# Kernel optimization log

Measured on AMD Instinct MI355X. Metric: run time of the kernel, lower is better.

Reference implementation:

```python
import jax, jax.numpy as jnp
import numpy as np

H = 8  # num_heads
C = 512  # embed_dims
L = 3  # num_layers
SCALE = (C // H) ** -0.5


def _ln(x, g, b, eps=1e-5):
    mu = jnp.mean(x, axis=-1, keepdims=True)
    var = jnp.mean((x - mu) ** 2, axis=-1, keepdims=True)
    return g * (x - mu) / jnp.sqrt(var + eps) + b


def setup_inputs() -> dict:
    key = jax.random.key(0)
    ks = jax.random.split(key, 12)
    B, Nq, Nk = 16, 64, 4096
    s = 0.02
    return dict(
        queries=jax.random.normal(ks[0], (B, Nq, C), jnp.float32),
        feat=jax.random.normal(ks[1], (B, Nk, C), jnp.float32),
        extra_token=jax.random.normal(ks[2], (B, 1, C), jnp.float32),
        Wq=jax.random.normal(ks[3], (L, C, C), jnp.float32) * s,
        bq=jnp.zeros((L, C), jnp.float32),
        Wk=jax.random.normal(ks[4], (L, C, C), jnp.float32) * s,
        bk=jnp.zeros((L, C), jnp.float32),
        Wv=jax.random.normal(ks[5], (L, C, C), jnp.float32) * s,
        bv=jnp.zeros((L, C), jnp.float32),
        Wo=jax.random.normal(ks[6], (L, C, C), jnp.float32) * s,
        bo=jnp.zeros((L, C), jnp.float32),
        W1=jax.random.normal(ks[7], (L, C, 4 * C), jnp.float32) * s,
        b1=jnp.zeros((L, 4 * C), jnp.float32),
        W2=jax.random.normal(ks[8], (L, 4 * C, C), jnp.float32) * s,
        b2=jnp.zeros((L, C), jnp.float32),
        g2=jnp.ones((L, C), jnp.float32),
        beta2=jnp.zeros((L, C), jnp.float32),
        g3=jnp.ones((L, C), jnp.float32),
        beta3=jnp.zeros((L, C), jnp.float32),
    )


def reference(queries, feat, extra_token, Wq, bq, Wk, bk, Wv, bv, Wo, bo,
              W1, b1, W2, b2, g2, beta2, g3, beta3):
    B, Nq, _ = queries.shape
    Nk = feat.shape[1]
    hd = C // H
    # extra gating token is NOT projected through q: raw reshape -> [B,H,1,hd]
    eq = extra_token.reshape(B, 1, H, hd).transpose(0, 2, 1, 3)
    x = queries
    outs, attns, affs = [], [], []
    for i in range(L):
        q = (x @ Wq[i] + bq[i]).reshape(B, Nq, H, hd).transpose(0, 2, 1, 3)
        k = (feat @ Wk[i] + bk[i]).reshape(B, Nk, H, hd).transpose(0, 2, 1, 3)
        v = (feat @ Wv[i] + bv[i]).reshape(B, Nk, H, hd).transpose(0, 2, 1, 3)
        attn = jnp.einsum('bhqd,bhkd->bhqk', q, k) * SCALE  # pre-softmax scores
        # affinity gate from extra token, averaged over heads -> [B,1,1,Nk]
        aff = jax.nn.sigmoid(jnp.mean(
            jnp.einsum('bhod,bhkd->bhok', eq, k) * SCALE, axis=1, keepdims=True))
        p = aff * jax.nn.softmax(attn, axis=-1)  # gated probabilities
        o = jnp.einsum('bhqk,bhkd->bqhd', p, v).reshape(B, Nq, C)
        o = o @ Wo[i] + bo[i]
        x = _ln(x + o, g2[i], beta2[i])
        ff = jax.nn.relu(x @ W1[i] + b1[i]) @ W2[i] + b2[i]
        x = _ln(x + ff, g3[i], beta3[i])
        outs.append(x)
        attns.append(attn.sum(axis=1) / H)  # head-averaged pre-softmax scores
        affs.append(aff)
    return (jnp.stack(outs), jnp.stack(attns), jnp.stack(affs))
```

## Files before the change

kernel.cpp:

```cpp
#include <hip/hip_runtime.h>


typedef unsigned short u16;
typedef __attribute__((ext_vector_type(8))) short short8;
typedef __attribute__((ext_vector_type(4))) short short4v;
typedef __attribute__((ext_vector_type(4))) float f32x4;

__device__ __forceinline__ float b2f(u16 u) {
    union { unsigned int i; float f; } v; v.i = ((unsigned int)u) << 16; return v.f;
}
__device__ __forceinline__ u16 f2b(float f) {
    unsigned int x = __float_as_uint(f);
    x += 0x7fffu + ((x >> 16) & 1u);
    return (u16)(x >> 16);
}

__device__ __forceinline__ float waveSum(float v) {
#pragma unroll
    for (int o = 32; o > 0; o >>= 1) v += __shfl_xor(v, o);
    return v;
}
__device__ __forceinline__ float waveMax(float v) {
#pragma unroll
    for (int o = 32; o > 0; o >>= 1) v = fmaxf(v, __shfl_xor(v, o));
    return v;
}

__device__ __forceinline__ void gl_lds16(const void* g, void* l) {
    __builtin_amdgcn_global_load_lds(
        (__attribute__((address_space(1))) void*)g,
        (__attribute__((address_space(3))) void*)l, 16, 0, 0);
}

template<bool BIAS_ROW, bool AFFC>
__global__ __launch_bounds__(512, 1) void gemm256_bt_k(
    const u16* __restrict__ A, const u16* __restrict__ Bt,
    const float* __restrict__ bias, u16* __restrict__ Cout,
    int lda, int ldb, int ldc, long sA2, long sB2, long sC2,
    const float* __restrict__ affc)
{
    __shared__ u16 As[3][256][64];
    __shared__ u16 Bs[3][128][64];
    const int t = threadIdx.x;
    const int lane = t & 63;
    const int wave = t >> 6;
    const int z = blockIdx.z;
    A  += (long)z * sA2;
    Bt += (long)z * sB2;
    const long cbase = (long)z * sC2;
    const int n0 = blockIdx.x * 128;
    const int m0 = blockIdx.y * 256;
    const int wm = wave >> 1;
    const int wn = wave & 1;
    const int rl = lane & 15, uq = lane >> 4;
    const int srow = lane >> 3;
    const int up   = lane & 7;

    f32x4 acc[4][4];
#pragma unroll
    for (int i = 0; i < 4; ++i)
#pragma unroll
        for (int j = 0; j < 4; ++j) acc[i][j] = (f32x4){0.f, 0.f, 0.f, 0.f};

    auto stage = [&](int buf, int kt) {
        const int k0 = kt * 64;
#pragma unroll
        for (int r = 0; r < 4; ++r) {
            const int row = r * 64 + wave * 8 + srow;
            const int ul = up ^ (row & 7);
            gl_lds16(A + (long)(m0 + row) * lda + k0 + ul * 8,
                     &As[buf][r * 64 + wave * 8][0]);
        }
#pragma unroll
        for (int r = 0; r < 2; ++r) {
            const int row = r * 64 + wave * 8 + srow;
            const int ul = up ^ (row & 7);
            gl_lds16(Bt + (long)(n0 + row) * ldb + k0 + ul * 8,
                     &Bs[buf][r * 64 + wave * 8][0]);
        }
    };

    auto compute = [&](int buf) {
        short8 af[2][4], bf[2][4];
#pragma unroll
        for (int kc = 0; kc < 2; ++kc) {
#pragma unroll
            for (int i = 0; i < 4; ++i) {
                const int R = wm * 64 + i * 16 + rl;
                af[kc][i] = *(const short8*)(&As[buf][R][((kc * 4 + uq) ^ (R & 7)) * 8]);
            }
#pragma unroll
            for (int j = 0; j < 4; ++j) {
                const int R = wn * 64 + j * 16 + rl;
                bf[kc][j] = *(const short8*)(&Bs[buf][R][((kc * 4 + uq) ^ (R & 7)) * 8]);
            }
        }
        __builtin_amdgcn_s_setprio(1);
#pragma unroll
        for (int kc = 0; kc < 2; ++kc)
#pragma unroll
            for (int i = 0; i < 4; ++i)
#pragma unroll
                for (int j = 0; j < 4; ++j)
                    acc[i][j] = __builtin_amdgcn_mfma_f32_16x16x32_bf16(
                        af[kc][i], bf[kc][j], acc[i][j], 0, 0, 0);
        __builtin_amdgcn_s_setprio(0);
    };

    stage(0, 0);
    stage(1, 1);
    asm volatile("s_waitcnt vmcnt(6)\n\ts_barrier" ::: "memory");

#pragma unroll
    for (int kt = 0; kt < 8; ++kt) {
        if (kt + 2 < 8) stage((kt + 2) % 3, kt + 2);
        compute(kt % 3);
        if (kt < 6) {
            asm volatile("s_waitcnt vmcnt(6)\n\ts_barrier" ::: "memory");
        } else if (kt == 6) {
            asm volatile("s_waitcnt vmcnt(0)\n\ts_barrier" ::: "memory");
        }
    }

    const int r0 = (lane >> 4) * 4;
    const int c0 = lane & 15;
#pragma unroll
    for (int i = 0; i < 4; ++i) {
#pragma unroll
        for (int j = 0; j < 4; ++j) {
#pragma unroll
            for (int r = 0; r < 4; ++r) {
                const int row = m0 + wm * 64 + i * 16 + r0 + r;
                const int col = n0 + wn * 64 + j * 16 + c0;
                float v = acc[i][j][r];
                if constexpr (BIAS_ROW) v += bias[row]; else v += bias[col];
                if constexpr (AFFC) v *= affc[(long)z * 4096 + col];
                Cout[cbase + (long)row * ldc + col] = f2b(v);
            }
        }
    }
}

template<int TM, int TN, bool OUT_BF16, bool RELU, bool BIAS_ROW, bool HAS_BIAS,
         bool AFFC, bool SMAX>
__global__ __launch_bounds__(256) void gemm_bt_k(
    const u16* __restrict__ A, const u16* __restrict__ Bt,
    const float* __restrict__ bias, void* __restrict__ Cout,
    int K, int lda, int ldb, int ldc,
    int bdiv, long sA1, long sA2, long sB1, long sB2, long sC1, long sC2,
    float alpha, const float* __restrict__ affc, const float2* __restrict__ stats)
{
    __shared__ u16 As[TM][64];
    __shared__ u16 Bs[TN][64];
    const int t = threadIdx.x;
    const int lane = t & 63;
    const int wave = t >> 6;
    const int z = blockIdx.z;
    const int zq = z / bdiv, zr = z % bdiv;
    A  += (long)zq * sA1 + (long)zr * sA2;
    Bt += (long)zq * sB1 + (long)zr * sB2;
    const long cbase = (long)zq * sC1 + (long)zr * sC2;
    const int n0 = blockIdx.x * TN;
    const int m0 = blockIdx.y * TM;
    constexpr int FM = TM / 32, FN = TN / 32;
    const int wr = wave >> 1, wc = wave & 1;
    const int rl = lane & 15, uq = lane >> 4;

    float2 st[FM];
    if constexpr (SMAX) {
#pragma unroll
        for (int i = 0; i < FM; ++i)
            st[i] = stats[zr * 64 + m0 + wr * (TM / 2) + i * 16 + rl];
    }

    f32x4 acc[FM][FN];
#pragma unroll
    for (int i = 0; i < FM; ++i)
#pragma unroll
        for (int j = 0; j < FN; ++j) acc[i][j] = (f32x4){0.f, 0.f, 0.f, 0.f};

    const int srow = lane >> 3;
    const int up   = lane & 7;

    for (int k0 = 0; k0 < K; k0 += 64) {
        __syncthreads();
#pragma unroll
        for (int r = 0; r < TM / 32; ++r) {
            const int br = (wave * (TM / 32) + r) * 8;
            const int row = br + srow;
            const int ul = up ^ (row & 7);
            gl_lds16(A + (long)(m0 + row) * lda + k0 + ul * 8, &As[br][0]);
        }
#pragma unroll
        for (int r = 0; r < TN / 32; ++r) {
            const int br = (wave * (TN / 32) + r) * 8;
            const int row = br + srow;
            const int ul = up ^ (row & 7);
            gl_lds16(Bt + (long)(n0 + row) * ldb + k0 + ul * 8, &Bs[br][0]);
        }
        __syncthreads();

#pragma unroll
        for (int kc = 0; kc < 2; ++kc) {
            short8 af[FM], bf[FN];
#pragma unroll
            for (int i = 0; i < FM; ++i) {
                const int R = wr * (TM / 2) + i * 16 + rl;
                af[i] = *(const short8*)(&As[R][((kc * 4 + uq) ^ (R & 7)) * 8]);
                if constexpr (SMAX) {
#pragma unroll
                    for (int e = 0; e < 8; ++e)
                        af[i][e] = (short)f2b(
                            __expf(b2f((u16)af[i][e]) - st[i].x) * st[i].y);
                }
            }
#pragma unroll
            for (int j = 0; j < FN; ++j) {
                const int R = wc * (TN / 2) + j * 16 + rl;
                bf[j] = *(const short8*)(&Bs[R][((kc * 4 + uq) ^ (R & 7)) * 8]);
            }
#pragma unroll
            for (int i = 0; i < FM; ++i)
#pragma unroll
                for (int j = 0; j < FN; ++j)
                    acc[i][j] = __builtin_amdgcn_mfma_f32_16x16x32_bf16(
                        af[i], bf[j], acc[i][j], 0, 0, 0);
        }
    }

    const int r0 = (lane >> 4) * 4;
    const int c0 = lane & 15;
#pragma unroll
    for (int i = 0; i < FM; ++i) {
#pragma unroll
        for (int j = 0; j < FN; ++j) {
#pragma unroll
            for (int r = 0; r < 4; ++r) {
                const int row = m0 + wr * (TM / 2) + i * 16 + r0 + r;
                const int col = n0 + wc * (TN / 2) + j * 16 + c0;
                float v = acc[i][j][r] * alpha;
                if constexpr (HAS_BIAS) {
                    if constexpr (BIAS_ROW) v += bias[row]; else v += bias[col];
                }
                if constexpr (AFFC) v *= affc[(long)zq * 4096 + col];
                if constexpr (RELU) v = fmaxf(v, 0.f);
                const long idx = cbase + (long)row * ldc + col;
                if constexpr (OUT_BF16) ((u16*)Cout)[idx] = f2b(v);
                else                    ((float*)Cout)[idx] = v;
            }
        }
    }
}

__global__ __launch_bounds__(256) void smstats_k(
    const u16* __restrict__ S, float2* __restrict__ stats,
    float* __restrict__ attns)
{
    const int bq = blockIdx.x;
    const int b = bq >> 6, q = bq & 63;
    const int t = threadIdx.x;
    const int w = t >> 6, lane = t & 63;
    __shared__ float red[4];
    const int kb = t * 16;

    float attnacc[16];
#pragma unroll
    for (int j = 0; j < 16; ++j) attnacc[j] = 0.f;

    for (int h = 0; h < 8; ++h) {
        const long roff = (((long)(b * 8 + h)) * 64 + q) * 4096;
        const u16* Srow = S + roff;
        float v[16];
        short8 s0 = *(const short8*)(Srow + kb);
        short8 s1 = *(const short8*)(Srow + kb + 8);
#pragma unroll
        for (int j = 0; j < 8; ++j) { v[j] = b2f((u16)s0[j]); v[8 + j] = b2f((u16)s1[j]); }

        float m = -3.0e38f;
#pragma unroll
        for (int j = 0; j < 16; ++j) m = fmaxf(m, v[j]);
        m = waveMax(m);
        __syncthreads();
        if (lane == 0) red[w] = m;
        __syncthreads();
        m = fmaxf(fmaxf(red[0], red[1]), fmaxf(red[2], red[3]));

        float s = 0.f;
#pragma unroll
        for (int j = 0; j < 16; ++j) s += __expf(v[j] - m);
        s = waveSum(s);
        __syncthreads();
        if (lane == 0) red[w] = s;
        __syncthreads();
        s = red[0] + red[1] + red[2] + red[3];

        if (t == 0) stats[(b * 8 + h) * 64 + q] = make_float2(m, 1.f / s);
#pragma unroll
        for (int j = 0; j < 16; ++j) attnacc[j] += v[j];
    }
    float* arow = attns + (long)bq * 4096;
#pragma unroll
    for (int j = 0; j < 16; ++j) arow[kb + j] = attnacc[j] * 0.125f;
}

__global__ __launch_bounds__(256) void pv_reduce_k(
    const float* __restrict__ part, u16* __restrict__ o16)
{
    const int i = blockIdx.x * 256 + threadIdx.x;
    const int d4 = i & 15;
    const int q  = (i >> 4) & 63;
    const int bh = i >> 10;
    const float* p = part + (long)bh * 4096 + q * 64 + d4 * 4;
    float4 s = {0.f, 0.f, 0.f, 0.f};
#pragma unroll
    for (int sp = 0; sp < 8; ++sp) {
        const float4 v = *(const float4*)(p + (long)sp * 524288);
        s.x += v.x; s.y += v.y; s.z += v.z; s.w += v.w;
    }
    const int b = bh >> 3, h = bh & 7;
    u16* o = o16 + (long)b * 32768 + q * 512 + h * 64 + d4 * 4;
    short4v r;
    r[0] = (short)f2b(s.x); r[1] = (short)f2b(s.y);
    r[2] = (short)f2b(s.z); r[3] = (short)f2b(s.w);
    *(short4v*)o = r;
}

__global__ __launch_bounds__(256) void ffred_k(
    const float* __restrict__ part, const float* __restrict__ bias,
    float* __restrict__ out)
{
    const int i = (blockIdx.x * 256 + threadIdx.x) * 4;
    const int c = i & 511;
    float4 s = *(const float4*)(part + i);
#pragma unroll
    for (int sp = 1; sp < 4; ++sp) {
        const float4 v = *(const float4*)(part + (long)sp * 524288 + i);
        s.x += v.x; s.y += v.y; s.z += v.z; s.w += v.w;
    }
    s.x += bias[c]; s.y += bias[c + 1]; s.z += bias[c + 2]; s.w += bias[c + 3];
    *(float4*)(out + i) = s;
}

__global__ __launch_bounds__(256) void umat_k(
    const float* __restrict__ Wk, const float* __restrict__ extra,
    float* __restrict__ u)
{
    __shared__ float ex[16][512];
    const int l = blockIdx.x;
    const int t = threadIdx.x;
    for (int i = t; i < 16 * 512 / 4; i += 256)
        ((float4*)&ex[0][0])[i] = ((const float4*)extra)[i];
    __syncthreads();
    const int lane = t & 63, wave = t >> 6;
    const int row = blockIdx.y * 4 + wave;
    const float* wrow = Wk + ((size_t)l * 512 + row) * 512 + lane * 8;
    float w[8];
#pragma unroll
    for (int j = 0; j < 8; ++j) w[j] = wrow[j];
    float s[16];
#pragma unroll
    for (int b = 0; b < 16; ++b) {
        float x = 0.f;
#pragma unroll
        for (int j = 0; j < 8; ++j) x += w[j] * ex[b][lane * 8 + j];
        s[b] = waveSum(x);
    }
    if (lane < 16) u[((size_t)l * 16 + lane) * 512 + row] = s[lane];
}

__global__ __launch_bounds__(256) void cbk_k(
    const float* __restrict__ bk, const float* __restrict__ extra,
    float* __restrict__ cb)
{
    const int gw = blockIdx.x * 4 + (threadIdx.x >> 6);
    const int lane = threadIdx.x & 63;
    const int l = gw >> 4, b = gw & 15;
    float s = 0.f;
#pragma unroll
    for (int j = 0; j < 8; ++j)
        s += extra[b * 512 + lane * 8 + j] * bk[l * 512 + lane * 8 + j];
    s = waveSum(s);
    if (lane == 0) cb[gw] = s;
}

__global__ __launch_bounds__(256) void cvt16_aff_k(
    const float* __restrict__ feat, u16* __restrict__ dst,
    const float* __restrict__ u, const float* __restrict__ cb,
    float* __restrict__ affb, float* __restrict__ affs_out)
{
    const int t = blockIdx.x * 256 + threadIdx.x;
    const long i = (long)t * 8;
    const int lane = threadIdx.x & 63;
    const int r = t >> 6;
    const int b = r >> 12;
    const float4 a0 = *(const float4*)(feat + i);
    const float4 a1 = *(const float4*)(feat + i + 4);
    short8 o;
    o[0] = (short)f2b(a0.x); o[1] = (short)f2b(a0.y);
    o[2] = (short)f2b(a0.z); o[3] = (short)f2b(a0.w);
    o[4] = (short)f2b(a1.x); o[5] = (short)f2b(a1.y);
    o[6] = (short)f2b(a1.z); o[7] = (short)f2b(a1.w);
    *(short8*)(dst + i) = o;
    const float f[8] = {a0.x, a0.y, a0.z, a0.w, a1.x, a1.y, a1.z, a1.w};
#pragma unroll
    for (int l = 0; l < 3; ++l) {
        const float* ur = u + ((size_t)l * 16 + b) * 512 + lane * 8;
        float s = 0.f;
#pragma unroll
        for (int j = 0; j < 8; ++j) s += f[j] * ur[j];
        s = waveSum(s);
        if (lane == 0) {
            const float av = 1.f / (1.f + __expf(-0.015625f * (s + cb[l * 16 + b])));
            affb[l * 65536 + r] = av;
            affs_out[l * 65536 + r] = av;
        }
    }
}

template<bool WRITE_OUT>
__global__ __launch_bounds__(256) void ln_k(
    float* __restrict__ x, const float* __restrict__ add,
    const float* __restrict__ g, const float* __restrict__ be,
    u16* __restrict__ x16, float* __restrict__ outp)
{
    const int r = blockIdx.x, t = threadIdx.x;
    const int w = t >> 6, lane = t & 63;
    __shared__ float red[4];
    float* xr = x + (long)r * 512;
    const float* ar = add + (long)r * 512;
    const float v0 = xr[2 * t]     + ar[2 * t];
    const float v1 = xr[2 * t + 1] + ar[2 * t + 1];
    float s = waveSum(v0 + v1);
    if (lane == 0) red[w] = s;
    __syncthreads();
    s = red[0] + red[1] + red[2] + red[3];
    const float mu = s * (1.f / 512.f);
    const float d0 = v0 - mu, d1 = v1 - mu;
    __syncthreads();
    float vs = waveSum(d0 * d0 + d1 * d1);
    if (lane == 0) red[w] = vs;
    __syncthreads();
    vs = red[0] + red[1] + red[2] + red[3];
    const float rs = rsqrtf(vs * (1.f / 512.f) + 1e-5f);
    const float o0 = g[2 * t]     * d0 * rs + be[2 * t];
    const float o1 = g[2 * t + 1] * d1 * rs + be[2 * t + 1];
    xr[2 * t] = o0; xr[2 * t + 1] = o1;
    x16[(long)r * 512 + 2 * t]     = f2b(o0);
    x16[(long)r * 512 + 2 * t + 1] = f2b(o1);
    if constexpr (WRITE_OUT) {
        outp[(long)r * 512 + 2 * t]     = o0;
        outp[(long)r * 512 + 2 * t + 1] = o1;
    }
}

__global__ __launch_bounds__(256) void initx_k(
    const float* __restrict__ src, float* __restrict__ x, u16* __restrict__ x16)
{
    const long i = ((long)blockIdx.x * 256 + threadIdx.x) * 8;
    const float4 a = *(const float4*)(src + i);
    const float4 b = *(const float4*)(src + i + 4);
    *(float4*)(x + i) = a;
    *(float4*)(x + i + 4) = b;
    short8 r;
    r[0] = (short)f2b(a.x); r[1] = (short)f2b(a.y); r[2] = (short)f2b(a.z); r[3] = (short)f2b(a.w);
    r[4] = (short)f2b(b.x); r[5] = (short)f2b(b.y); r[6] = (short)f2b(b.z); r[7] = (short)f2b(b.w);
    *(short8*)(x16 + i) = r;
}

__global__ __launch_bounds__(256) void transpose_w_k(
    const float* __restrict__ W, u16* __restrict__ WT, int K, int N)
{
    __shared__ float tile[32][33];
    const int z = blockIdx.z;
    W  += (size_t)z * K * N;
    WT += (size_t)z * K * N;
    const int n0 = blockIdx.x * 32, k0 = blockIdx.y * 32;
    const int tx = threadIdx.x & 31, ty = threadIdx.x >> 5;
#pragma unroll
    for (int j = 0; j < 32; j += 8)
        tile[ty + j][tx] = W[(size_t)(k0 + ty + j) * N + n0 + tx];
    __syncthreads();
#pragma unroll
    for (int j = 0; j < 32; j += 8)
        WT[(size_t)(n0 + ty + j) * K + k0 + tx] = f2b(tile[tx][ty + j]);
}

extern "C" void kernel_launch(void* const* d_in, const int* in_sizes, int n_in,
                              void* d_out, int out_size, void* d_ws, size_t ws_size,
                              hipStream_t stream)
{
    (void)in_sizes; (void)n_in; (void)out_size; (void)ws_size;
    const float* queries = (const float*)d_in[0];
    const float* feat    = (const float*)d_in[1];
    const float* extra   = (const float*)d_in[2];
    const float* Wq = (const float*)d_in[3];  const float* bq = (const float*)d_in[4];
    const float* Wk = (const float*)d_in[5];  const float* bk = (const float*)d_in[6];
    const float* Wv = (const float*)d_in[7];  const float* bv = (const float*)d_in[8];
    const float* Wo = (const float*)d_in[9];  const float* bo = (const float*)d_in[10];
    const float* W1 = (const float*)d_in[11]; const float* b1 = (const float*)d_in[12];
    const float* W2 = (const float*)d_in[13]; const float* b2 = (const float*)d_in[14];
    const float* g2 = (const float*)d_in[15]; const float* be2 = (const float*)d_in[16];
    const float* g3 = (const float*)d_in[17]; const float* be3 = (const float*)d_in[18];

    char* wsb = (char*)d_ws;
    size_t off = 0;
    auto alloc = [&](size_t bytes) -> char* {
        char* p = wsb + off; off += (bytes + 255) & ~(size_t)255; return p;
    };
    u16*  feat16 = (u16*)alloc(33554432ull * 2);
    u16*  WqT = (u16*)alloc(786432ull * 2);
    u16*  WkT = (u16*)alloc(786432ull * 2);
    u16*  WvT = (u16*)alloc(786432ull * 2);
    u16*  WoT = (u16*)alloc(786432ull * 2);
    u16*  W1T = (u16*)alloc(3145728ull * 2);
    u16*  W2T = (u16*)alloc(3145728ull * 2);
    u16*  K16 = (u16*)alloc(33554432ull * 2);
    u16*  VT16 = (u16*)alloc(33554432ull * 2);
    u16*  q16 = (u16*)alloc(524288ull * 2);
    u16*  S16 = (u16*)alloc(33554432ull * 2);
    float* affb  = (float*)alloc(196608ull * 4);
    u16*  o16 = (u16*)alloc(524288ull * 2);
    float* oproj = (float*)alloc(524288ull * 4);
    float* xb    = (float*)alloc(524288ull * 4);
    u16*  x16 = (u16*)alloc(524288ull * 2);
    u16*  h116 = (u16*)alloc(2097152ull * 2);
    float* ffb   = (float*)alloc(524288ull * 4);
    float* uvec  = (float*)alloc(24576ull * 4);
    float* cb    = (float*)alloc(48ull * 4);
    float2* stats = (float2*)alloc(8192ull * 8);
    float* partPV = (float*)K16;
    float* part2  = (float*)VT16;

    float* out_f = (float*)d_out;
    float* outs_base  = out_f;
    float* attns_base = out_f + 1572864;
    float* affs_base  = out_f + 14155776;

    umat_k<<<dim3(3, 128), 256, 0, stream>>>(Wk, extra, uvec);
    cbk_k<<<12, 256, 0, stream>>>(bk, extra, cb);
    cvt16_aff_k<<<16384, 256, 0, stream>>>(feat, feat16, uvec, cb, affb, affs_base);
    initx_k<<<256, 256, 0, stream>>>(queries, xb, x16);
    transpose_w_k<<<dim3(16, 16, 3), 256, 0, stream>>>(Wq, WqT, 512, 512);
    transpose_w_k<<<dim3(16, 16, 3), 256, 0, stream>>>(Wk, WkT, 512, 512);
    transpose_w_k<<<dim3(16, 16, 3), 256, 0, stream>>>(Wv, WvT, 512, 512);
    transpose_w_k<<<dim3(16, 16, 3), 256, 0, stream>>>(Wo, WoT, 512, 512);
    transpose_w_k<<<dim3(64, 16, 3), 256, 0, stream>>>(W1, W1T, 512, 2048);
    transpose_w_k<<<dim3(16, 64, 3), 256, 0, stream>>>(W2, W2T, 2048, 512);

    for (int i = 0; i < 3; ++i) {
        gemm256_bt_k<false, false><<<dim3(4, 256, 1), 512, 0, stream>>>(
            feat16, WkT + i * 262144, bk + i * 512, K16,
            512, 512, 512, 0, 0, 0, nullptr);
        gemm256_bt_k<true, true><<<dim3(32, 2, 16), 512, 0, stream>>>(
            WvT + i * 262144, feat16, bv + i * 512, VT16,
            512, 512, 4096, 0, 2097152, 2097152, affb + i * 65536);
        gemm_bt_k<64, 64, true, false, false, true, false, false>
            <<<dim3(8, 16, 1), 256, 0, stream>>>(
            x16, WqT + i * 262144, bq + i * 512, q16,
            512, 512, 512, 512, 1, 0, 0, 0, 0, 0, 0, 1.f, nullptr, nullptr);
        gemm_bt_k<64, 128, true, false, false, false, false, false>
            <<<dim3(32, 1, 128), 256, 0, stream>>>(
            q16, K16, nullptr, S16,
            64, 512, 512, 4096, 8, 32768, 64, 2097152, 64, 2097152, 262144,
            0.125f, nullptr, nullptr);
        smstats_k<<<1024, 256, 0, stream>>>(
            S16, stats, attns_base + (size_t)i * 4194304);
        gemm_bt_k<64, 64, false, false, false, false, false, true>
            <<<dim3(1, 1, 1024), 256, 0, stream>>>(
            S16, VT16, nullptr, partPV,
            512, 4096, 4096, 64, 128, 512, 262144, 512, 262144, 524288, 4096,
            1.f, nullptr, stats);
        pv_reduce_k<<<512, 256, 0, stream>>>(partPV, o16);
        gemm_bt_k<64, 64, false, false, false, true, false, false>
            <<<dim3(8, 16, 1), 256, 0, stream>>>(
            o16, WoT + i * 262144, bo + i * 512, oproj,
            512, 512, 512, 512, 1, 0, 0, 0, 0, 0, 0, 1.f, nullptr, nullptr);
        ln_k<false><<<1024, 256, 0, stream>>>(xb, oproj, g2 + i * 512, be2 + i * 512, x16, nullptr);
        gemm_bt_k<64, 128, true, true, false, true, false, false>
            <<<dim3(16, 16, 1), 256, 0, stream>>>(
            x16, W1T + (size_t)i * 1048576, b1 + i * 2048, h116,
            512, 512, 512, 2048, 1, 0, 0, 0, 0, 0, 0, 1.f, nullptr, nullptr);
        gemm_bt_k<64, 64, false, false, false, false, false, false>
            <<<dim3(8, 16, 4), 256, 0, stream>>>(
            h116, W2T + (size_t)i * 1048576, nullptr, part2,
            512, 2048, 2048, 512, 1, 512, 0, 512, 0, 524288, 0,
            1.f, nullptr, nullptr);
        ffred_k<<<512, 256, 0, stream>>>(part2, b2 + i * 512, ffb);
        ln_k<true><<<1024, 256, 0, stream>>>(xb, ffb, g3 + i * 512, be3 + i * 512, x16,
                                             outs_base + (size_t)i * 524288);
    }
}
```

Baseline: 816.9 us.

## Enlarge K/V projection GEMM tiles to 256x256 with XCD-aware block remapping

Grows the large K and V projection GEMM output tile from 256x128 to 256x256, with each wave computing a 128x64 sub-tile, so each loaded A/B slice gets more reuse. Pipelining drops from a triple-buffered, partially waited scheme to plain double buffering with __syncthreads, keeping LDS within budget. Block IDs are remapped so that consecutive tiles land on the same XCD, aiming for better L2 locality. In exchange there are more accumulator registers, half as many workgroups, and less latency hiding from the shallower prefetch.

After: 777.3 us. 1.05x faster.

```diff
diff --git a/kernel.cpp b/kernel.cpp
--- a/kernel.cpp
+++ b/kernel.cpp
@@ -32,33 +32,46 @@
         (__attribute__((address_space(3))) void*)l, 16, 0, 0);
 }
 
-template<bool BIAS_ROW, bool AFFC>
-__global__ __launch_bounds__(512, 1) void gemm256_bt_k(
+template<bool BIAS_ROW, bool HAS_BIAS, bool AFFC>
+__global__ __launch_bounds__(512, 1) void gemm256x256_k(
     const u16* __restrict__ A, const u16* __restrict__ Bt,
     const float* __restrict__ bias, u16* __restrict__ Cout,
     int lda, int ldb, int ldc, long sA2, long sB2, long sC2,
     const float* __restrict__ affc)
 {
-    __shared__ u16 As[3][256][64];
-    __shared__ u16 Bs[3][128][64];
+    __shared__ u16 As[2][256][64];
+    __shared__ u16 Bs[2][256][64];
     const int t = threadIdx.x;
     const int lane = t & 63;
     const int wave = t >> 6;
-    const int z = blockIdx.z;
+
+    const int gx = gridDim.x, gy = gridDim.y;
+    const int nwg = gx * gy * gridDim.z;
+    int id;
+    {
+        const int orig = blockIdx.x + blockIdx.y * gx + blockIdx.z * gx * gy;
+        const int qq = nwg >> 3, rr = nwg & 7;
+        const int xcd = orig & 7, sub = orig >> 3;
+        id = (xcd < rr ? xcd * (qq + 1) : rr * (qq + 1) + (xcd - rr) * qq) + sub;
+    }
+    const int bx = id % gx;
+    const int by = (id / gx) % gy;
+    const int z  = id / (gx * gy);
+
     A  += (long)z * sA2;
     Bt += (long)z * sB2;
     const long cbase = (long)z * sC2;
-    const int n0 = blockIdx.x * 128;
-    const int m0 = blockIdx.y * 256;
-    const int wm = wave >> 1;
-    const int wn = wave & 1;
+    const int n0 = bx * 256;
+    const int m0 = by * 256;
+    const int wm = wave >> 2;
+    const int wn = wave & 3;
     const int rl = lane & 15, uq = lane >> 4;
     const int srow = lane >> 3;
     const int up   = lane & 7;
 
-    f32x4 acc[4][4];
-#pragma unroll
-    for (int i = 0; i < 4; ++i)
+    f32x4 acc[8][4];
+#pragma unroll
+    for (int i = 0; i < 8; ++i)
 #pragma unroll
         for (int j = 0; j < 4; ++j) acc[i][j] = (f32x4){0.f, 0.f, 0.f, 0.f};
 
@@ -72,7 +85,7 @@
                      &As[buf][r * 64 + wave * 8][0]);
         }
 #pragma unroll
-        for (int r = 0; r < 2; ++r) {
+        for (int r = 0; r < 4; ++r) {
             const int row = r * 64 + wave * 8 + srow;
             const int ul = up ^ (row & 7);
             gl_lds16(Bt + (long)(n0 + row) * ldb + k0 + ul * 8,
@@ -81,59 +94,55 @@
     };
 
     auto compute = [&](int buf) {
-        short8 af[2][4], bf[2][4];
 #pragma unroll
         for (int kc = 0; kc < 2; ++kc) {
-#pragma unroll
-            for (int i = 0; i < 4; ++i) {
-                const int R = wm * 64 + i * 16 + rl;
-                af[kc][i] = *(const short8*)(&As[buf][R][((kc * 4 + uq) ^ (R & 7)) * 8]);
+            short8 af[8], bf[4];
+#pragma unroll
+            for (int i = 0; i < 8; ++i) {
+                const int R = wm * 128 + i * 16 + rl;
+                af[i] = *(const short8*)(&As[buf][R][((kc * 4 + uq) ^ (R & 7)) * 8]);
             }
 #pragma unroll
             for (int j = 0; j < 4; ++j) {
                 const int R = wn * 64 + j * 16 + rl;
-                bf[kc][j] = *(const short8*)(&Bs[buf][R][((kc * 4 + uq) ^ (R & 7)) * 8]);
+                bf[j] = *(const short8*)(&Bs[buf][R][((kc * 4 + uq) ^ (R & 7)) * 8]);
             }
-        }
-        __builtin_amdgcn_s_setprio(1);
-#pragma unroll
-        for (int kc = 0; kc < 2; ++kc)
-#pragma unroll
-            for (int i = 0; i < 4; ++i)
+            __builtin_amdgcn_s_setprio(1);
+#pragma unroll
+            for (int i = 0; i < 8; ++i)
 #pragma unroll
                 for (int j = 0; j < 4; ++j)
                     acc[i][j] = __builtin_amdgcn_mfma_f32_16x16x32_bf16(
-                        af[kc][i], bf[kc][j], acc[i][j], 0, 0, 0);
-        __builtin_amdgcn_s_setprio(0);
+                        af[i], bf[j], acc[i][j], 0, 0, 0);
+            __builtin_amdgcn_s_setprio(0);
+        }
     };
 
     stage(0, 0);
-    stage(1, 1);
-    asm volatile("s_waitcnt vmcnt(6)\n\ts_barrier" ::: "memory");
-
+    __syncthreads();
+    int buf = 0;
 #pragma unroll
     for (int kt = 0; kt < 8; ++kt) {
-        if (kt + 2 < 8) stage((kt + 2) % 3, kt + 2);
-        compute(kt % 3);
-        if (kt < 6) {
-            asm volatile("s_waitcnt vmcnt(6)\n\ts_barrier" ::: "memory");
-        } else if (kt == 6) {
-            asm volatile("s_waitcnt vmcnt(0)\n\ts_barrier" ::: "memory");
-        }
+        if (kt + 1 < 8) stage(buf ^ 1, kt + 1);
+        compute(buf);
+        __syncthreads();
+        buf ^= 1;
     }
 
     const int r0 = (lane >> 4) * 4;
     const int c0 = lane & 15;
 #pragma unroll
-    for (int i = 0; i < 4; ++i) {
+    for (int i = 0; i < 8; ++i) {
 #pragma unroll
         for (int j = 0; j < 4; ++j) {
 #pragma unroll
             for (int r = 0; r < 4; ++r) {
-                const int row = m0 + wm * 64 + i * 16 + r0 + r;
+                const int row = m0 + wm * 128 + i * 16 + r0 + r;
                 const int col = n0 + wn * 64 + j * 16 + c0;
                 float v = acc[i][j][r];
-                if constexpr (BIAS_ROW) v += bias[row]; else v += bias[col];
+                if constexpr (HAS_BIAS) {
+                    if constexpr (BIAS_ROW) v += bias[row]; else v += bias[col];
+                }
                 if constexpr (AFFC) v *= affc[(long)z * 4096 + col];
                 Cout[cbase + (long)row * ldc + col] = f2b(v);
             }
@@ -548,10 +557,10 @@
     transpose_w_k<<<dim3(16, 64, 3), 256, 0, stream>>>(W2, W2T, 2048, 512);
 
     for (int i = 0; i < 3; ++i) {
-        gemm256_bt_k<false, false><<<dim3(4, 256, 1), 512, 0, stream>>>(
+        gemm256x256_k<false, true, false><<<dim3(2, 256, 1), 512, 0, stream>>>(
             feat16, WkT + i * 262144, bk + i * 512, K16,
             512, 512, 512, 0, 0, 0, nullptr);
-        gemm256_bt_k<true, true><<<dim3(32, 2, 16), 512, 0, stream>>>(
+        gemm256x256_k<true, true, true><<<dim3(16, 2, 16), 512, 0, stream>>>(
             WvT + i * 262144, feat16, bv + i * 512, VT16,
             512, 512, 4096, 0, 2097152, 2097152, affb + i * 65536);
         gemm_bt_k<64, 64, true, false, false, true, false, false>
```
